# Kernel tuning notes

Hardware: AMD Instinct MI355X
Metric: run time of the kernel (lower is better)

Reference implementation:

```python
import jax, jax.numpy as jnp
import numpy as np

LAMBDA1 = 0.3366
LAMBDA2 = 0.2424
LAMBDA3 = 0.06
LR = 0.1
N_ITERS = 10          # fixed iteration count standing in for the eps-based while loop
BETA1, BETA2, ADAM_EPS = 0.9, 0.999, 1e-8


def setup_inputs() -> dict:
    key = jax.random.key(0)
    k1, k2, k3 = jax.random.split(key, 3)
    D, T, K = 512, 50000, 16
    return {
        "embedding": jax.random.normal(k1, (D, T), jnp.float32),
        "basis_init": jax.random.normal(k2, (D, K), jnp.float32),
        "activation_init": jax.random.normal(k3, (K, T), jnp.float32),
        "k": K,
    }


def _matrix_l1(X):
    # torch.linalg.norm(X, ord=1) on a 2D tensor = induced 1-norm = max column abs-sum
    return jnp.max(jnp.sum(jnp.abs(X), axis=0))


def _jitter(A):
    # temporal jitter penalty: sum of abs frame-to-frame differences
    return jnp.sum(jnp.abs(A[:, 1:] - A[:, :-1]))


def _shrink(X):
    # faithful to the (buggy) torch _shrink: sign(X) * max(0, |X - lr*l|)
    return jnp.sign(X) * jnp.maximum(0.0, jnp.abs(X - LR * LAMBDA1))


def _adam(p, g, m, v, t):
    m = BETA1 * m + (1.0 - BETA1) * g
    v = BETA2 * v + (1.0 - BETA2) * g * g
    mh = m / (1.0 - BETA1 ** t)
    vh = v / (1.0 - BETA2 ** t)
    p = p - LR * mh / (jnp.sqrt(vh) + ADAM_EPS)
    return p, m, v


def _run(embedding, basis_init, activation_init):
    A = activation_init  # optimizer_act.step() is never called in the source -> A is constant

    def loss_from_B(B):
        return (_matrix_l1(embedding - B @ A)
                + LAMBDA1 * _matrix_l1(B)
                + LAMBDA2 * _matrix_l1(A)
                + LAMBDA3 * _jitter(A))

    # iteration 1: loss is computed on the raw parameter (shrink applied after the step)
    P = basis_init
    m = jnp.zeros_like(P)
    v = jnp.zeros_like(P)
    g = jax.grad(loss_from_B)(P)
    P, m, v = _adam(P, g, m, v, jnp.float32(1.0))

    # iterations 2..N: loss sees shrink(P); gradient flows through the shrink into P
    def step(carry, t):
        P, m, v = carry
        g = jax.grad(lambda p: loss_from_B(_shrink(p)))(P)
        P, m, v = _adam(P, g, m, v, t)
        return (P, m, v), None

    ts = jnp.arange(2, N_ITERS + 1, dtype=jnp.float32)
    (P, m, v), _ = jax.lax.scan(step, (P, m, v), ts)
    return _shrink(P), A


def reference(embedding, basis_init, activation_init, k):
    # returns (embedding_basis_matrix, activation_matrix) as in OutputDiarization
    return _run(embedding, basis_init, activation_init)
```

## Files before the change

### kernel.cpp

```cpp
#include <hip/hip_runtime.h>

#define D 512
#define T 50000
#define T4 12500
#define K 16

#define S 32
#define RS (D / S)
#define CB 49

#define LAMBDA1 0.3366f
#define LR      0.1f
#define SHRINK_C (LR * LAMBDA1)
#define BETA1   0.9f
#define BETA2   0.999f
#define ADAM_EPS 1e-8f

__device__ __forceinline__ float sgn(float x) {
    return (x > 0.f) ? 1.f : ((x < 0.f) ? -1.f : 0.f);
}

__global__ void init_kernel(const float* __restrict__ Pin, float* __restrict__ P,
                            float* __restrict__ m, float* __restrict__ v,
                            float* __restrict__ B, unsigned long long* slot) {
    int idx = blockIdx.x * blockDim.x + threadIdx.x;
    if (idx < D * K) {
        float p = Pin[idx];
        P[idx] = p;
        m[idx] = 0.f;
        v[idx] = 0.f;
        B[idx] = p;
    }
    if (idx == 0) *slot = 0ull;
}

__global__ __launch_bounds__(256) void partial_colsum_kernel(
        const float* __restrict__ E, const float* __restrict__ A,
        const float* __restrict__ B, float4* __restrict__ partial4) {
    const int j4 = blockIdx.x * blockDim.x + threadIdx.x;
    const int s  = blockIdx.y;
    if (j4 >= T4) return;

    const float4* E4 = (const float4*)E;
    const float4* A4 = (const float4*)A;

    float4 a[K];
#pragma unroll
    for (int k = 0; k < K; ++k) a[k] = A4[k * T4 + j4];

    float4 acc = make_float4(0.f, 0.f, 0.f, 0.f);
    const int r0 = s * RS;
#pragma unroll 4
    for (int ii = 0; ii < RS; ++ii) {
        const int i = r0 + ii;
        const float* Br = B + i * K;
        float4 e = E4[i * T4 + j4];
#pragma unroll
        for (int k = 0; k < K; ++k) {
            const float bk = Br[k];
            e.x -= bk * a[k].x;
            e.y -= bk * a[k].y;
            e.z -= bk * a[k].z;
            e.w -= bk * a[k].w;
        }
        acc.x += fabsf(e.x);
        acc.y += fabsf(e.y);
        acc.z += fabsf(e.z);
        acc.w += fabsf(e.w);
    }
    partial4[s * T4 + j4] = acc;
}

__global__ __launch_bounds__(256) void reduce_argmax_kernel(
        const float4* __restrict__ partial4, unsigned long long* slot) {
    const int j4 = blockIdx.x * blockDim.x + threadIdx.x;
    unsigned long long key = 0ull;
    if (j4 < T4) {
        float4 sum = make_float4(0.f, 0.f, 0.f, 0.f);
#pragma unroll
        for (int ss = 0; ss < S; ++ss) {
            float4 p = partial4[ss * T4 + j4];
            sum.x += p.x; sum.y += p.y; sum.z += p.z; sum.w += p.w;
        }
        float best = sum.x; int jb = 4 * j4;
        if (sum.y > best) { best = sum.y; jb = 4 * j4 + 1; }
        if (sum.z > best) { best = sum.z; jb = 4 * j4 + 2; }
        if (sum.w > best) { best = sum.w; jb = 4 * j4 + 3; }
        key = (((unsigned long long)__float_as_uint(best)) << 32) | (unsigned int)jb;
    }
#pragma unroll
    for (int off = 32; off > 0; off >>= 1) {
        unsigned long long o = __shfl_down(key, off, 64);
        if (o > key) key = o;
    }
    __shared__ unsigned long long wmax[4];
    const int lane = threadIdx.x & 63, wid = threadIdx.x >> 6;
    if (lane == 0) wmax[wid] = key;
    __syncthreads();
    if (threadIdx.x == 0) {
        unsigned long long bk = wmax[0];
        for (int w = 1; w < 4; ++w)
            if (wmax[w] > bk) bk = wmax[w];
        atomicMax(slot, bk);
    }
}

__global__ __launch_bounds__(512) void update_kernel(
        const float* __restrict__ E, const float* __restrict__ A,
        float* __restrict__ B, float* __restrict__ P,
        float* __restrict__ m, float* __restrict__ v,
        unsigned long long* slot, float bias1, float bias2, int shrinkGrad) {
    int i = threadIdx.x;
    __shared__ float colB[K];
    __shared__ int js_s, ks_s;
    if (i < K) colB[i] = 0.f;
    if (i == 0) js_s = (int)((*slot) & 0xffffffffull);
    __syncthreads();
    int js = js_s;

    float b[K];
#pragma unroll
    for (int k = 0; k < K; ++k) b[k] = B[i * K + k];

    float r = E[i * T + js];
#pragma unroll
    for (int k = 0; k < K; ++k) r -= b[k] * A[k * T + js];
    float s = sgn(r);

#pragma unroll
    for (int k = 0; k < K; ++k) {
        float x = fabsf(b[k]);
#pragma unroll
        for (int off = 32; off > 0; off >>= 1) x += __shfl_down(x, off, 64);
        if ((threadIdx.x & 63) == 0) atomicAdd(&colB[k], x);
    }
    __syncthreads();
    if (i == 0) {
        int kb = 0;
        float best = colB[0];
        for (int k = 1; k < K; ++k)
            if (colB[k] > best) { best = colB[k]; kb = k; }
        ks_s = kb;
        *slot = 0ull;
    }
    __syncthreads();
    int ks = ks_s;

#pragma unroll
    for (int k = 0; k < K; ++k) {
        float g = -s * A[k * T + js];
        if (k == ks) g += LAMBDA1 * sgn(b[k]);
        float p = P[i * K + k];
        if (shrinkGrad) g *= sgn(p) * sgn(p - SHRINK_C);
        float mm = BETA1 * m[i * K + k] + (1.f - BETA1) * g;
        float vv = BETA2 * v[i * K + k] + (1.f - BETA2) * g * g;
        m[i * K + k] = mm;
        v[i * K + k] = vv;
        p -= LR * (mm / bias1) / (sqrtf(vv / bias2) + ADAM_EPS);
        P[i * K + k] = p;
        B[i * K + k] = sgn(p) * fmaxf(0.f, fabsf(p - SHRINK_C));
    }
}

__global__ void output_kernel(const float* __restrict__ B, const float* __restrict__ A,
                              float4* __restrict__ out) {
    int idx = blockIdx.x * blockDim.x + threadIdx.x;
    const int nB4 = (D * K) / 4;
    const int nTot4 = (D * K + K * T) / 4;
    if (idx < nB4) {
        out[idx] = ((const float4*)B)[idx];
    } else if (idx < nTot4) {
        out[idx] = ((const float4*)A)[idx - nB4];
    }
}

extern "C" void kernel_launch(void* const* d_in, const int* in_sizes, int n_in,
                              void* d_out, int out_size, void* d_ws, size_t ws_size,
                              hipStream_t stream) {
    const float* E   = (const float*)d_in[0];
    const float* Bin = (const float*)d_in[1];
    const float* A   = (const float*)d_in[2];

    float* P = (float*)d_ws;
    float* m = P + D * K;
    float* v = m + D * K;
    float* B = v + D * K;
    unsigned long long* slot = (unsigned long long*)(B + D * K);
    float4* partial4 = (float4*)(slot + 2);

    init_kernel<<<(D * K + 255) / 256, 256, 0, stream>>>(Bin, P, m, v, B, slot);

    for (int it = 1; it <= 10; ++it) {
        partial_colsum_kernel<<<dim3(CB, S), 256, 0, stream>>>(E, A, B, partial4);
        reduce_argmax_kernel<<<CB, 256, 0, stream>>>(partial4, slot);
        float b1 = 1.f - powf(BETA1, (float)it);
        float b2 = 1.f - powf(BETA2, (float)it);
        update_kernel<<<1, 512, 0, stream>>>(E, A, B, P, m, v, slot, b1, b2,
                                             (it >= 2) ? 1 : 0);
    }

    const int nTot4 = (D * K + K * T) / 4;
    output_kernel<<<(nTot4 + 255) / 256, 256, 0, stream>>>(B, A, (float4*)d_out);
}
```

Baseline: 789.7 us.

## Fuse column-sum and argmax into one kernel with in-block row-group reduction

Replaces the two-kernel partial column sum plus global reduce with a single kernel in which each block covers 16 float4 columns and splits the 512 rows across 16 row groups, then reduces through LDS before a block-level atomicMax. This removes the partial-sum buffer round-trip through global memory and one launch per iteration. B is staged in LDS, E is read with batched nontemporal loads, and the block count becomes about 782. Each block now loads all of B into LDS, a redundant cost, and each E row access covers only 256 bytes, which may hurt coalescing.

```diff
diff --git a/kernel.cpp b/kernel.cpp
--- a/kernel.cpp
+++ b/kernel.cpp
@@ -5,9 +5,10 @@
 #define T4 12500
 #define K 16
 
-#define S 32
-#define RS (D / S)
-#define CB 49
+#define COLS 16
+#define RGS 16
+#define RPT (D / RGS)
+#define NBLK ((T4 + COLS - 1) / COLS)
 
 #define LAMBDA1 0.3366f
 #define LR      0.1f
@@ -15,6 +16,8 @@
 #define BETA1   0.9f
 #define BETA2   0.999f
 #define ADAM_EPS 1e-8f
+
+typedef float vfloat4 __attribute__((ext_vector_type(4)));
 
 __device__ __forceinline__ float sgn(float x) {
     return (x > 0.f) ? 1.f : ((x < 0.f) ? -1.f : 0.f);
@@ -34,74 +37,84 @@
     if (idx == 0) *slot = 0ull;
 }
 
-__global__ __launch_bounds__(256) void partial_colsum_kernel(
+__global__ __launch_bounds__(256) void colsum_argmax_kernel(
         const float* __restrict__ E, const float* __restrict__ A,
-        const float* __restrict__ B, float4* __restrict__ partial4) {
-    const int j4 = blockIdx.x * blockDim.x + threadIdx.x;
-    const int s  = blockIdx.y;
-    if (j4 >= T4) return;
-
-    const float4* E4 = (const float4*)E;
-    const float4* A4 = (const float4*)A;
-
-    float4 a[K];
-#pragma unroll
-    for (int k = 0; k < K; ++k) a[k] = A4[k * T4 + j4];
-
-    float4 acc = make_float4(0.f, 0.f, 0.f, 0.f);
-    const int r0 = s * RS;
-#pragma unroll 4
-    for (int ii = 0; ii < RS; ++ii) {
-        const int i = r0 + ii;
-        const float* Br = B + i * K;
-        float4 e = E4[i * T4 + j4];
-#pragma unroll
-        for (int k = 0; k < K; ++k) {
-            const float bk = Br[k];
-            e.x -= bk * a[k].x;
-            e.y -= bk * a[k].y;
-            e.z -= bk * a[k].z;
-            e.w -= bk * a[k].w;
+        const float* __restrict__ B, unsigned long long* slot) {
+    const int tid = threadIdx.x;
+    const int col = tid & (COLS - 1);
+    const int rg  = tid >> 4;
+    const int j4  = blockIdx.x * COLS + col;
+    const bool active = (j4 < T4);
+
+    const vfloat4* E4 = (const vfloat4*)E;
+    const vfloat4* A4 = (const vfloat4*)A;
+    const vfloat4* B4 = (const vfloat4*)B;
+
+    __shared__ vfloat4 ldsB[D * K / 4];
+    __shared__ vfloat4 ldsAcc[RGS][COLS];
+
+#pragma unroll
+    for (int u = 0; u < (D * K / 4) / 256; ++u)
+        ldsB[tid + 256 * u] = B4[tid + 256 * u];
+    __syncthreads();
+
+    vfloat4 acc = (vfloat4)(0.f);
+    if (active) {
+        vfloat4 a[K];
+#pragma unroll
+        for (int k = 0; k < K; ++k) a[k] = A4[k * T4 + j4];
+
+        const int r0 = rg * RPT;
+        for (int base = 0; base < RPT; base += 8) {
+            vfloat4 eb[8];
+#pragma unroll
+            for (int u = 0; u < 8; ++u)
+                eb[u] = __builtin_nontemporal_load(&E4[(r0 + base + u) * T4 + j4]);
+#pragma unroll
+            for (int u = 0; u < 8; ++u) {
+                const vfloat4* Br4 = &ldsB[(r0 + base + u) * (K / 4)];
+                vfloat4 e = eb[u];
+#pragma unroll
+                for (int q = 0; q < K / 4; ++q) {
+                    const vfloat4 b4 = Br4[q];
+                    e -= b4.x * a[4*q+0];
+                    e -= b4.y * a[4*q+1];
+                    e -= b4.z * a[4*q+2];
+                    e -= b4.w * a[4*q+3];
+                }
+                acc.x += fabsf(e.x);
+                acc.y += fabsf(e.y);
+                acc.z += fabsf(e.z);
+                acc.w += fabsf(e.w);
+            }
         }
-        acc.x += fabsf(e.x);
-        acc.y += fabsf(e.y);
-        acc.z += fabsf(e.z);
-        acc.w += fabsf(e.w);
-    }
-    partial4[s * T4 + j4] = acc;
-}
-
-__global__ __launch_bounds__(256) void reduce_argmax_kernel(
-        const float4* __restrict__ partial4, unsigned long long* slot) {
-    const int j4 = blockIdx.x * blockDim.x + threadIdx.x;
-    unsigned long long key = 0ull;
-    if (j4 < T4) {
-        float4 sum = make_float4(0.f, 0.f, 0.f, 0.f);
-#pragma unroll
-        for (int ss = 0; ss < S; ++ss) {
-            float4 p = partial4[ss * T4 + j4];
-            sum.x += p.x; sum.y += p.y; sum.z += p.z; sum.w += p.w;
+    }
+    ldsAcc[rg][col] = acc;
+    __syncthreads();
+
+    if (tid < 64) {
+        unsigned long long key = 0ull;
+        if (tid < COLS) {
+            vfloat4 tot = ldsAcc[0][tid];
+#pragma unroll
+            for (int g = 1; g < RGS; ++g)
+                tot += ldsAcc[g][tid];
+            const int j4b = blockIdx.x * COLS + tid;
+            if (j4b < T4) {
+                float best = tot.x; int jb = 4 * j4b;
+                if (tot.y > best) { best = tot.y; jb = 4 * j4b + 1; }
+                if (tot.z > best) { best = tot.z; jb = 4 * j4b + 2; }
+                if (tot.w > best) { best = tot.w; jb = 4 * j4b + 3; }
+                key = (((unsigned long long)__float_as_uint(best)) << 32)
+                      | (unsigned int)jb;
+            }
         }
-        float best = sum.x; int jb = 4 * j4;
-        if (sum.y > best) { best = sum.y; jb = 4 * j4 + 1; }
-        if (sum.z > best) { best = sum.z; jb = 4 * j4 + 2; }
-        if (sum.w > best) { best = sum.w; jb = 4 * j4 + 3; }
-        key = (((unsigned long long)__float_as_uint(best)) << 32) | (unsigned int)jb;
-    }
-#pragma unroll
-    for (int off = 32; off > 0; off >>= 1) {
-        unsigned long long o = __shfl_down(key, off, 64);
-        if (o > key) key = o;
-    }
-    __shared__ unsigned long long wmax[4];
-    const int lane = threadIdx.x & 63, wid = threadIdx.x >> 6;
-    if (lane == 0) wmax[wid] = key;
-    __syncthreads();
-    if (threadIdx.x == 0) {
-        unsigned long long bk = wmax[0];
-        for (int w = 1; w < 4; ++w)
-            if (wmax[w] > bk) bk = wmax[w];
-        atomicMax(slot, bk);
+#pragma unroll
+        for (int off = 8; off > 0; off >>= 1) {
+            unsigned long long o = __shfl_down(key, off, 64);
+            if (o > key) key = o;
+        }
+        if (tid == 0) atomicMax(slot, key);
     }
 }
 
@@ -186,13 +199,11 @@
     float* v = m + D * K;
     float* B = v + D * K;
     unsigned long long* slot = (unsigned long long*)(B + D * K);
-    float4* partial4 = (float4*)(slot + 2);
 
     init_kernel<<<(D * K + 255) / 256, 256, 0, stream>>>(Bin, P, m, v, B, slot);
 
     for (int it = 1; it <= 10; ++it) {
-        partial_colsum_kernel<<<dim3(CB, S), 256, 0, stream>>>(E, A, B, partial4);
-        reduce_argmax_kernel<<<CB, 256, 0, stream>>>(partial4, slot);
+        colsum_argmax_kernel<<<NBLK, 256, 0, stream>>>(E, A, B, slot);
         float b1 = 1.f - powf(BETA1, (float)it);
         float b2 = 1.f - powf(BETA2, (float)it);
         update_kernel<<<1, 512, 0, stream>>>(E, A, B, P, m, v, slot, b1, b2,
```

Measured after the change: 785.1 us. Within noise of the previous version (-0.6%).
